# Performance work log

Hardware: AMD Instinct MI355X
Metric: run time of the kernel (lower is better)

The kernel has to match this reference:

```python
import jax, jax.numpy as jnp
import numpy as np

N = 50000      # nodes
E = 1600000    # edges (before self loops)
F = 128        # input_dim
H = 4          # num_heads
D = 32         # hidden_dim (per head)
B = 16         # graphs in batch
NEG_SLOPE = 0.2  # PyG GATv2Conv default negative_slope


def setup_inputs() -> dict:
    key = jax.random.key(0)
    ks = jax.random.split(key, 8)
    x = jax.random.normal(ks[0], (N, F), dtype=jnp.float32)
    edge_index = jax.random.randint(ks[1], (2, E), 0, N, dtype=jnp.int32)
    batch = jnp.sort(jax.random.randint(ks[2], (N,), 0, B, dtype=jnp.int32))
    s = 0.05
    W_l = jax.random.normal(ks[3], (F, H * D), dtype=jnp.float32) * s
    b_l = jnp.zeros((H * D,), dtype=jnp.float32)
    W_r = jax.random.normal(ks[4], (F, H * D), dtype=jnp.float32) * s
    b_r = jnp.zeros((H * D,), dtype=jnp.float32)
    att = jax.random.normal(ks[5], (H, D), dtype=jnp.float32) * s
    bias = jnp.zeros((H * D,), dtype=jnp.float32)
    return {"x": x, "edge_index": edge_index, "batch": batch,
            "W_l": W_l, "b_l": b_l, "W_r": W_r, "b_r": b_r,
            "att": att, "bias": bias}


def reference(x, edge_index, batch, W_l, b_l, W_r, b_r, att, bias):
    n = x.shape[0]
    # PyG GATv2Conv adds self loops by default
    loops = jnp.arange(n, dtype=edge_index.dtype)
    src = jnp.concatenate([edge_index[0], loops])  # message source j
    dst = jnp.concatenate([edge_index[1], loops])  # message target i

    xl = (x @ W_l + b_l).reshape(n, H, D)  # source transform
    xr = (x @ W_r + b_r).reshape(n, H, D)  # target transform

    # per-edge GATv2 attention logits: a^T LeakyReLU(xl_j + xr_i)
    m = xl[src] + xr[dst]                                   # [E+N, H, D]
    e = jnp.sum(jax.nn.leaky_relu(m, NEG_SLOPE) * att, -1)  # [E+N, H]

    # softmax over incoming edges of each destination node
    e_max = jax.ops.segment_max(e, dst, num_segments=n)
    ex = jnp.exp(e - e_max[dst])
    den = jax.ops.segment_sum(ex, dst, num_segments=n)
    alpha = ex / den[dst]                                   # [E+N, H]

    # weighted scatter-sum aggregation of source features
    out = jax.ops.segment_sum(alpha[..., None] * xl[src], dst, num_segments=n)
    out = out.reshape(n, H * D) + bias                      # concat heads + bias
    out = jax.nn.relu(out)

    # global max pool over nodes of each graph
    pooled = jax.ops.segment_max(out, batch, num_segments=B)
    pooled = jnp.where(jnp.isfinite(pooled), pooled, 0.0)   # guard empty graphs
    return pooled
```

## Files before the change

kernel.cpp:

```cpp
#include <hip/hip_runtime.h>

#define NN 50000
#define NE 1600000
#define FDIM 128
#define CDIM 128
#define NGRAPH 16
#define SLOPE 0.2f
#define CSTRIDE 96
#define BINSH 7
#define NBIN 391
#define EPB 6400
#define NB1 250
#define EPT 25
#define CAP 5120
#define POOL_NODES 64
#define POOL_NB ((NN + POOL_NODES - 1) / POOL_NODES)
#define TNB 782

__device__ __forceinline__ unsigned short f2bf(float f) {
    unsigned u = __float_as_uint(f);
    return (unsigned short)((u + 0x7FFFu + ((u >> 16) & 1u)) >> 16);
}
__device__ __forceinline__ unsigned packbf(float a, float b) {
    return (unsigned)f2bf(a) | ((unsigned)f2bf(b) << 16);
}
#define BFLO(u) __uint_as_float((u) << 16)
#define BFHI(u) __uint_as_float((u) & 0xffff0000u)

typedef __attribute__((ext_vector_type(8))) short short8;
typedef __attribute__((ext_vector_type(4))) float f32x4;
union FragU { uint4 u; short8 s; };

__global__ __launch_bounds__(256) void k_init(float* __restrict__ out,
                                              int* __restrict__ gbin_cnt) {
    int i = blockIdx.x * 256 + threadIdx.x;
    if (i < NGRAPH * CDIM) out[i] = 0.f;
    if (i < NBIN) gbin_cnt[i] = 0;
}

__global__ __launch_bounds__(256) void k_front(
    const float* __restrict__ x,
    const float* __restrict__ Wl, const float* __restrict__ bl,
    const float* __restrict__ Wr, const float* __restrict__ br,
    const int* __restrict__ src, const int* __restrict__ dst,
    int* __restrict__ gbin_cnt, unsigned* __restrict__ gstage,
    unsigned short* __restrict__ xlh, float* __restrict__ xr) {
    __shared__ __align__(16) char shraw[32768];
    const int tid = threadIdx.x;

    if (blockIdx.x < NB1) {
        int* bcnt = (int*)shraw;
        int* boff = bcnt + NBIN;
        int* gb   = boff + NBIN;
        int* sc   = gb + NBIN;
        unsigned* st = (unsigned*)(sc + 256);
        const int t  = tid;
        const int e0 = blockIdx.x * EPB;

        for (int b = t; b < NBIN; b += 256) bcnt[b] = 0;
        __syncthreads();

        unsigned sd[EPT]; int bn[EPT]; int pl[EPT];
#pragma unroll
        for (int k = 0; k < EPT; k++) {
            int e = e0 + k * 256 + t;
            int s = src[e], d = dst[e];
            bn[k] = d >> BINSH;
            sd[k] = (unsigned)s | ((unsigned)(d & 127) << 16)
                                | ((unsigned)bn[k] << 23);
            pl[k] = atomicAdd(&bcnt[bn[k]], 1);
        }
        __syncthreads();

        int c0 = (2*t     < NBIN) ? bcnt[2*t]     : 0;
        int c1 = (2*t + 1 < NBIN) ? bcnt[2*t + 1] : 0;
        int v  = c0 + c1;
        sc[t] = v; __syncthreads();
        for (int off = 1; off < 256; off <<= 1) {
            int add = (t >= off) ? sc[t - off] : 0;
            __syncthreads();
            sc[t] += add;
            __syncthreads();
        }
        int base = sc[t] - v;
        if (2*t     < NBIN) boff[2*t]     = base;
        if (2*t + 1 < NBIN) boff[2*t + 1] = base + c0;
        __syncthreads();

        for (int b = t; b < NBIN; b += 256) {
            int c = bcnt[b];
            gb[b] = (c > 0) ? atomicAdd(&gbin_cnt[b], c) : 0;
        }
#pragma unroll
        for (int k = 0; k < EPT; k++) st[boff[bn[k]] + pl[k]] = sd[k];
        __syncthreads();

        for (int idx = t; idx < EPB; idx += 256) {
            unsigned w = st[idx];
            int b = w >> 23;
            int p = gb[b] + (idx - boff[b]);
            if (p < CAP) gstage[(size_t)b * CAP + p] = w;
        }
    } else {
        uint4* wfrag = (uint4*)shraw;
        const int bid   = blockIdx.x - NB1;
        const int wv    = tid >> 6;
        const int lane  = tid & 63;
        const int quad  = lane >> 4;
        const int col   = lane & 15;
        const int node0 = bid * 64;
        const int nodeA = node0 + wv * 16 + col;
        const bool aval = nodeA < NN;

        FragU afrag[4];
#pragma unroll
        for (int kq = 0; kq < 4; kq++) {
            float4 lo = make_float4(0.f,0.f,0.f,0.f), hi = lo;
            if (aval) {
                const float* ap = &x[(size_t)nodeA * FDIM + kq * 32 + quad * 8];
                lo = *(const float4*)ap;
                hi = *(const float4*)(ap + 4);
            }
            afrag[kq].u.x = packbf(lo.x, lo.y);
            afrag[kq].u.y = packbf(lo.z, lo.w);
            afrag[kq].u.z = packbf(hi.x, hi.y);
            afrag[kq].u.w = packbf(hi.z, hi.w);
        }

        const int myrow0 = node0 + wv * 16 + quad * 4;

        for (int mat = 0; mat < 2; mat++) {
            const float* W  = mat ? Wr : Wl;
            const float* bb = mat ? br : bl;
            __syncthreads();
            for (int i = 0; i < 8; i++) {
                int C = i * 256 + tid;
                int ccol = C & 15, cq = (C >> 4) & 3, ckq = (C >> 6) & 3, cnt_ = C >> 8;
                const float* wp = &W[(size_t)(ckq * 32 + cq * 8) * CDIM + cnt_ * 16 + ccol];
                uint4 u;
                u.x = packbf(wp[0],        wp[CDIM]);
                u.y = packbf(wp[2*CDIM],   wp[3*CDIM]);
                u.z = packbf(wp[4*CDIM],   wp[5*CDIM]);
                u.w = packbf(wp[6*CDIM],   wp[7*CDIM]);
                wfrag[C] = u;
            }
            __syncthreads();

#pragma unroll
            for (int nt = 0; nt < 8; nt++) {
                f32x4 acc = {0.f, 0.f, 0.f, 0.f};
#pragma unroll
                for (int kq = 0; kq < 4; kq++) {
                    FragU bfr;
                    bfr.u = wfrag[(nt * 4 + kq) * 64 + lane];
                    acc = __builtin_amdgcn_mfma_f32_16x16x32_bf16(
                              afrag[kq].s, bfr.s, acc, 0, 0, 0);
                }
                int ch = nt * 16 + col;
                float bv = bb[ch];
                if (mat == 0) {
#pragma unroll
                    for (int r = 0; r < 4; r++) {
                        int node = myrow0 + r;
                        if (node < NN)
                            xlh[(size_t)node * CDIM + ch] = f2bf(acc[r] + bv);
                    }
                } else {
#pragma unroll
                    for (int r = 0; r < 4; r++) {
                        int node = myrow0 + r;
                        if (node < NN)
                            xr[(size_t)node * CDIM + ch] = acc[r] + bv;
                    }
                }
            }
        }
    }
}

__global__ __launch_bounds__(256) void k_csr(
    const int* __restrict__ gbin_cnt, const unsigned* __restrict__ gstage,
    int* __restrict__ cnt, unsigned short* __restrict__ colp) {
    __shared__ int nfill[128];
    __shared__ unsigned short crow[128 * CSTRIDE];
    const int bin = blockIdx.x;
    const int t   = threadIdx.x;
    const int n0  = bin << BINSH;
    const int nb  = min(128, NN - n0);
    const int m   = min(gbin_cnt[bin], CAP);

    if (t < 128) nfill[t] = 0;
    __syncthreads();

    for (int i = t; i < m; i += 256) {
        unsigned w = gstage[(size_t)bin * CAP + i];
        int dl = (w >> 16) & 127;
        int p  = atomicAdd(&nfill[dl], 1);
        if (p < CSTRIDE - 1) crow[dl * CSTRIDE + p] = (unsigned short)(w & 0xFFFF);
    }
    __syncthreads();

    if (t < nb) {
        int c = min(nfill[t], CSTRIDE - 1);
        crow[t * CSTRIDE + c] = (unsigned short)(n0 + t);
        cnt[n0 + t] = c + 1;
    }
    __syncthreads();

    unsigned* gout = (unsigned*)colp + (size_t)bin * (128 * CSTRIDE / 2);
    const unsigned* cin = (const unsigned*)crow;
    for (int idx = t; idx < 128 * CSTRIDE / 2; idx += 256) gout[idx] = cin[idx];
}

__device__ __forceinline__ void edge_body(
    const unsigned short* __restrict__ xlh, int j, int ch0,
    const float4& rx0, const float4& rx1,
    const float4& p0, const float4& p1,
    const float4& q0, const float4& q1,
    float& s, float* acc) {
    uint4 q = *(const uint4*)&xlh[(size_t)j * CDIM + ch0];
    float4 v0 = make_float4(BFLO(q.x), BFHI(q.x), BFLO(q.y), BFHI(q.y));
    float4 v1 = make_float4(BFLO(q.z), BFHI(q.z), BFLO(q.w), BFHI(q.w));
    float t0, d = 0.f;
    t0 = v0.x + rx0.x; d = fmaf(t0, p0.x, d); d = fmaf(fabsf(t0), q0.x, d);
    t0 = v0.y + rx0.y; d = fmaf(t0, p0.y, d); d = fmaf(fabsf(t0), q0.y, d);
    t0 = v0.z + rx0.z; d = fmaf(t0, p0.z, d); d = fmaf(fabsf(t0), q0.z, d);
    t0 = v0.w + rx0.w; d = fmaf(t0, p0.w, d); d = fmaf(fabsf(t0), q0.w, d);
    t0 = v1.x + rx1.x; d = fmaf(t0, p1.x, d); d = fmaf(fabsf(t0), q1.x, d);
    t0 = v1.y + rx1.y; d = fmaf(t0, p1.y, d); d = fmaf(fabsf(t0), q1.y, d);
    t0 = v1.z + rx1.z; d = fmaf(t0, p1.z, d); d = fmaf(fabsf(t0), q1.z, d);
    t0 = v1.w + rx1.w; d = fmaf(t0, p1.w, d); d = fmaf(fabsf(t0), q1.w, d);
    d += __shfl_xor(d, 1);
    d += __shfl_xor(d, 2);
    float w = __expf(d);
    s += w;
    acc[0] = fmaf(w, v0.x, acc[0]);
    acc[1] = fmaf(w, v0.y, acc[1]);
    acc[2] = fmaf(w, v0.z, acc[2]);
    acc[3] = fmaf(w, v0.w, acc[3]);
    acc[4] = fmaf(w, v1.x, acc[4]);
    acc[5] = fmaf(w, v1.y, acc[5]);
    acc[6] = fmaf(w, v1.z, acc[6]);
    acc[7] = fmaf(w, v1.w, acc[7]);
}

__global__ __launch_bounds__(256) void k_aggregate(
    const unsigned short* __restrict__ xlh, const float* __restrict__ xr,
    const float* __restrict__ att, const float* __restrict__ bias,
    const int* __restrict__ cnt, const unsigned short* __restrict__ colp,
    float* __restrict__ nodeout) {
    const int wave = blockIdx.x * 4 + (threadIdx.x >> 6);
    const int lane = threadIdx.x & 63;
    const int i     = wave;
    const size_t start = (size_t)i * CSTRIDE;
    const int deg   = cnt[i];
    const int grp   = lane >> 4;
    const int ch0   = (lane & 15) * 8;

    int cj0 = (int)colp[start + lane];
    int cj1 = 0;
    if (deg > 64) cj1 = (int)colp[start + 64 + lane];

    const float4 rx0 = *(const float4*)&xr[(size_t)i * CDIM + ch0];
    const float4 rx1 = *(const float4*)&xr[(size_t)i * CDIM + ch0 + 4];
    const float4 aa0 = *(const float4*)&att[ch0];
    const float4 aa1 = *(const float4*)&att[ch0 + 4];
    const float4 p0 = make_float4(0.6f*aa0.x, 0.6f*aa0.y, 0.6f*aa0.z, 0.6f*aa0.w);
    const float4 p1 = make_float4(0.6f*aa1.x, 0.6f*aa1.y, 0.6f*aa1.z, 0.6f*aa1.w);
    const float4 q0 = make_float4(0.4f*aa0.x, 0.4f*aa0.y, 0.4f*aa0.z, 0.4f*aa0.w);
    const float4 q1 = make_float4(0.4f*aa1.x, 0.4f*aa1.y, 0.4f*aa1.z, 0.4f*aa1.w);

    float s = 0.f;
    float acc[8];
#pragma unroll
    for (int k = 0; k < 8; k++) acc[k] = 0.f;

    const int full = deg >> 2;
    const int f0   = full < 16 ? full : 16;
#pragma unroll 2
    for (int t = 0; t < f0; t++) {
        int j = __shfl(cj0, t * 4 + grp);
        edge_body(xlh, j, ch0, rx0, rx1, p0, p1, q0, q1, s, acc);
    }
    for (int t = 16; t < full; t++) {
        int j = __shfl(cj1, t * 4 + grp - 64);
        edge_body(xlh, j, ch0, rx0, rx1, p0, p1, q0, q1, s, acc);
    }
    int e  = full * 4 + grp;
    int jt = (e < 64) ? __shfl(cj0, e) : __shfl(cj1, (e - 64) & 63);
    if (e < deg)
        edge_body(xlh, jt, ch0, rx0, rx1, p0, p1, q0, q1, s, acc);

#pragma unroll
    for (int dist = 16; dist <= 32; dist <<= 1) {
        s += __shfl_xor(s, dist);
#pragma unroll
        for (int k = 0; k < 8; k++) acc[k] += __shfl_xor(acc[k], dist);
    }

    if (grp == 0) {
        float inv = 1.f / s;
        float4 o0, o1;
        const float4 b0 = *(const float4*)&bias[ch0];
        const float4 b1 = *(const float4*)&bias[ch0 + 4];
        o0.x = fmaxf(fmaf(acc[0], inv, b0.x), 0.f);
        o0.y = fmaxf(fmaf(acc[1], inv, b0.y), 0.f);
        o0.z = fmaxf(fmaf(acc[2], inv, b0.z), 0.f);
        o0.w = fmaxf(fmaf(acc[3], inv, b0.w), 0.f);
        o1.x = fmaxf(fmaf(acc[4], inv, b1.x), 0.f);
        o1.y = fmaxf(fmaf(acc[5], inv, b1.y), 0.f);
        o1.z = fmaxf(fmaf(acc[6], inv, b1.z), 0.f);
        o1.w = fmaxf(fmaf(acc[7], inv, b1.w), 0.f);
        float* op = &nodeout[(size_t)i * CDIM + ch0];
        *(float4*)op       = o0;
        *(float4*)(op + 4) = o1;
    }
}

__global__ __launch_bounds__(256) void k_pool(
    const float* __restrict__ nodeout, const int* __restrict__ batch,
    float* __restrict__ out) {
    const int tid  = threadIdx.x;
    const int c4   = (tid & 31) * 4;
    const int nl   = tid >> 5;
    const int base = blockIdx.x * POOL_NODES;
    float4 mx = make_float4(0.f, 0.f, 0.f, 0.f);
    int cur = -1;
#pragma unroll
    for (int k = 0; k < POOL_NODES / 8; k++) {
        int node = base + k * 8 + nl;
        if (node >= NN) break;
        int g = batch[node];
        if (g != cur) {
            if (cur >= 0) {
                int* op = (int*)&out[cur * CDIM + c4];
                if (mx.x > 0.f) atomicMax(op,     __float_as_int(mx.x));
                if (mx.y > 0.f) atomicMax(op + 1, __float_as_int(mx.y));
                if (mx.z > 0.f) atomicMax(op + 2, __float_as_int(mx.z));
                if (mx.w > 0.f) atomicMax(op + 3, __float_as_int(mx.w));
            }
            cur = g;
            mx = make_float4(0.f, 0.f, 0.f, 0.f);
        }
        float4 v = *(const float4*)&nodeout[(size_t)node * CDIM + c4];
        mx.x = fmaxf(mx.x, v.x);
        mx.y = fmaxf(mx.y, v.y);
        mx.z = fmaxf(mx.z, v.z);
        mx.w = fmaxf(mx.w, v.w);
    }
    if (cur >= 0) {
        int* op = (int*)&out[cur * CDIM + c4];
        if (mx.x > 0.f) atomicMax(op,     __float_as_int(mx.x));
        if (mx.y > 0.f) atomicMax(op + 1, __float_as_int(mx.y));
        if (mx.z > 0.f) atomicMax(op + 2, __float_as_int(mx.z));
        if (mx.w > 0.f) atomicMax(op + 3, __float_as_int(mx.w));
    }
}

extern "C" void kernel_launch(void* const* d_in, const int* in_sizes, int n_in,
                              void* d_out, int out_size, void* d_ws, size_t ws_size,
                              hipStream_t stream) {
    const float* x     = (const float*)d_in[0];
    const int*   ei    = (const int*)d_in[1];
    const int*   batch = (const int*)d_in[2];
    const float* Wl    = (const float*)d_in[3];
    const float* bl    = (const float*)d_in[4];
    const float* Wr    = (const float*)d_in[5];
    const float* br    = (const float*)d_in[6];
    const float* att   = (const float*)d_in[7];
    const float* bias  = (const float*)d_in[8];
    float* out = (float*)d_out;

    char* w = (char*)d_ws;
    float*          xr       = (float*)w;          w += (size_t)NN * CDIM * 4;
    float*          nodeout  = (float*)w;          w += (size_t)NN * CDIM * 4;
    unsigned short* xlh      = (unsigned short*)w; w += (size_t)NN * CDIM * 2;
    int*            cnt      = (int*)w;            w += (size_t)NN * 4;
    unsigned short* colp     = (unsigned short*)w; w += (size_t)NBIN * 128 * CSTRIDE * 2;
    unsigned*       gstage   = (unsigned*)w;       w += (size_t)NBIN * CAP * 4;
    int*            gbin_cnt = (int*)w;            w += (size_t)NBIN * 4;

    const int* src = ei;
    const int* dst = ei + NE;

    k_init<<<10, 256, 0, stream>>>(out, gbin_cnt);
    k_front<<<NB1 + TNB, 256, 0, stream>>>(x, Wl, bl, Wr, br,
                                           src, dst, gbin_cnt, gstage, xlh, xr);
    k_csr<<<NBIN, 256, 0, stream>>>(gbin_cnt, gstage, cnt, colp);
    k_aggregate<<<NN / 4, 256, 0, stream>>>(xlh, xr, att, bias,
                                            cnt, colp, nodeout);
    k_pool<<<POOL_NB, 256, 0, stream>>>(nodeout, batch, out);
}
```

Before: 237.3 us.

## Fuse CSR build, attention aggregation and max-pool into one back-half kernel

Replaces the separate CSR, aggregate and pool kernels with one kernel. Each 512-thread block builds the adjacency for half of a 128-node bin in shared memory, then aggregates those nodes wave by wave and folds the ReLU outputs straight into per-graph max atomics. This drops the global round trips for the column list, degree counts and the full node-output matrix, along with two kernel launches. In exchange every bin's staging buffer is scanned twice, once per half, and each wave handles eight nodes serially, which gives fewer independent waves for hiding gather latency.

Result: slower. 318.2 us (+34.0%).

```diff
diff --git a/kernel.cpp b/kernel.cpp
--- a/kernel.cpp
+++ b/kernel.cpp
@@ -13,8 +13,6 @@
 #define NB1 250
 #define EPT 25
 #define CAP 5120
-#define POOL_NODES 64
-#define POOL_NB ((NN + POOL_NODES - 1) / POOL_NODES)
 #define TNB 782
 
 __device__ __forceinline__ unsigned short f2bf(float f) {
@@ -178,182 +176,190 @@
     }
 }
 
-__global__ __launch_bounds__(256) void k_csr(
+__global__ __launch_bounds__(512) void k_backhalf(
+    const unsigned short* __restrict__ xlh, const float* __restrict__ xr,
+    const float* __restrict__ att, const float* __restrict__ bias,
+    const int* __restrict__ batch,
     const int* __restrict__ gbin_cnt, const unsigned* __restrict__ gstage,
-    int* __restrict__ cnt, unsigned short* __restrict__ colp) {
-    __shared__ int nfill[128];
-    __shared__ unsigned short crow[128 * CSTRIDE];
-    const int bin = blockIdx.x;
-    const int t   = threadIdx.x;
-    const int n0  = bin << BINSH;
-    const int nb  = min(128, NN - n0);
+    float* __restrict__ out) {
+    __shared__ int nfill[64];
+    __shared__ unsigned short crow[64 * CSTRIDE];
+    const int bin = blockIdx.x >> 1;
+    const int h   = blockIdx.x & 1;
+    const int tid = threadIdx.x;
+    const int n0  = (bin << BINSH) + h * 64;
+    const int nb  = min(64, NN - n0);
     const int m   = min(gbin_cnt[bin], CAP);
 
-    if (t < 128) nfill[t] = 0;
+    if (tid < 64) nfill[tid] = 0;
     __syncthreads();
 
-    for (int i = t; i < m; i += 256) {
+    for (int i = tid; i < m; i += 512) {
         unsigned w = gstage[(size_t)bin * CAP + i];
         int dl = (w >> 16) & 127;
-        int p  = atomicAdd(&nfill[dl], 1);
-        if (p < CSTRIDE - 1) crow[dl * CSTRIDE + p] = (unsigned short)(w & 0xFFFF);
+        if ((dl >> 6) == h) {
+            int r = dl & 63;
+            int p = atomicAdd(&nfill[r], 1);
+            if (p < CSTRIDE - 1) crow[r * CSTRIDE + p] = (unsigned short)(w & 0xFFFF);
+        }
     }
     __syncthreads();
-
-    if (t < nb) {
-        int c = min(nfill[t], CSTRIDE - 1);
-        crow[t * CSTRIDE + c] = (unsigned short)(n0 + t);
-        cnt[n0 + t] = c + 1;
+    if (tid < nb) {
+        int c = min(nfill[tid], CSTRIDE - 1);
+        crow[tid * CSTRIDE + c] = (unsigned short)(n0 + tid);
+        nfill[tid] = c + 1;
     }
     __syncthreads();
 
-    unsigned* gout = (unsigned*)colp + (size_t)bin * (128 * CSTRIDE / 2);
-    const unsigned* cin = (const unsigned*)crow;
-    for (int idx = t; idx < 128 * CSTRIDE / 2; idx += 256) gout[idx] = cin[idx];
-}
-
-__device__ __forceinline__ void edge_body(
-    const unsigned short* __restrict__ xlh, int j, int ch0,
-    const float4& rx0, const float4& rx1,
-    const float4& p0, const float4& p1,
-    const float4& q0, const float4& q1,
-    float& s, float* acc) {
-    uint4 q = *(const uint4*)&xlh[(size_t)j * CDIM + ch0];
-    float4 v0 = make_float4(BFLO(q.x), BFHI(q.x), BFLO(q.y), BFHI(q.y));
-    float4 v1 = make_float4(BFLO(q.z), BFHI(q.z), BFLO(q.w), BFHI(q.w));
-    float t0, d = 0.f;
-    t0 = v0.x + rx0.x; d = fmaf(t0, p0.x, d); d = fmaf(fabsf(t0), q0.x, d);
-    t0 = v0.y + rx0.y; d = fmaf(t0, p0.y, d); d = fmaf(fabsf(t0), q0.y, d);
-    t0 = v0.z + rx0.z; d = fmaf(t0, p0.z, d); d = fmaf(fabsf(t0), q0.z, d);
-    t0 = v0.w + rx0.w; d = fmaf(t0, p0.w, d); d = fmaf(fabsf(t0), q0.w, d);
-    t0 = v1.x + rx1.x; d = fmaf(t0, p1.x, d); d = fmaf(fabsf(t0), q1.x, d);
-    t0 = v1.y + rx1.y; d = fmaf(t0, p1.y, d); d = fmaf(fabsf(t0), q1.y, d);
-    t0 = v1.z + rx1.z; d = fmaf(t0, p1.z, d); d = fmaf(fabsf(t0), q1.z, d);
-    t0 = v1.w + rx1.w; d = fmaf(t0, p1.w, d); d = fmaf(fabsf(t0), q1.w, d);
-    d += __shfl_xor(d, 1);
-    d += __shfl_xor(d, 2);
-    float w = __expf(d);
-    s += w;
-    acc[0] = fmaf(w, v0.x, acc[0]);
-    acc[1] = fmaf(w, v0.y, acc[1]);
-    acc[2] = fmaf(w, v0.z, acc[2]);
-    acc[3] = fmaf(w, v0.w, acc[3]);
-    acc[4] = fmaf(w, v1.x, acc[4]);
-    acc[5] = fmaf(w, v1.y, acc[5]);
-    acc[6] = fmaf(w, v1.z, acc[6]);
-    acc[7] = fmaf(w, v1.w, acc[7]);
-}
-
-__global__ __launch_bounds__(256) void k_aggregate(
-    const unsigned short* __restrict__ xlh, const float* __restrict__ xr,
-    const float* __restrict__ att, const float* __restrict__ bias,
-    const int* __restrict__ cnt, const unsigned short* __restrict__ colp,
-    float* __restrict__ nodeout) {
-    const int wave = blockIdx.x * 4 + (threadIdx.x >> 6);
-    const int lane = threadIdx.x & 63;
-    const int i     = wave;
-    const size_t start = (size_t)i * CSTRIDE;
-    const int deg   = cnt[i];
-    const int grp   = lane >> 4;
-    const int ch0   = (lane & 15) * 8;
-
-    int cj0 = (int)colp[start + lane];
-    int cj1 = 0;
-    if (deg > 64) cj1 = (int)colp[start + 64 + lane];
-
-    const float4 rx0 = *(const float4*)&xr[(size_t)i * CDIM + ch0];
-    const float4 rx1 = *(const float4*)&xr[(size_t)i * CDIM + ch0 + 4];
+    const int wv   = tid >> 6;
+    const int lane = tid & 63;
+    const int grp  = lane >> 4;
+    const int ch0  = (lane & 15) * 8;
+
     const float4 aa0 = *(const float4*)&att[ch0];
     const float4 aa1 = *(const float4*)&att[ch0 + 4];
     const float4 p0 = make_float4(0.6f*aa0.x, 0.6f*aa0.y, 0.6f*aa0.z, 0.6f*aa0.w);
     const float4 p1 = make_float4(0.6f*aa1.x, 0.6f*aa1.y, 0.6f*aa1.z, 0.6f*aa1.w);
     const float4 q0 = make_float4(0.4f*aa0.x, 0.4f*aa0.y, 0.4f*aa0.z, 0.4f*aa0.w);
     const float4 q1 = make_float4(0.4f*aa1.x, 0.4f*aa1.y, 0.4f*aa1.z, 0.4f*aa1.w);
-
-    float s = 0.f;
-    float acc[8];
-#pragma unroll
-    for (int k = 0; k < 8; k++) acc[k] = 0.f;
-
-    const int full = deg >> 2;
-    const int f0   = full < 16 ? full : 16;
+    const float4 b0 = *(const float4*)&bias[ch0];
+    const float4 b1 = *(const float4*)&bias[ch0 + 4];
+
+    float pmax[8];
+#pragma unroll
+    for (int k = 0; k < 8; k++) pmax[k] = 0.f;
+    int curg = -1;
+
+    for (int k = 0; k < 8; k++) {
+        int r = wv * 8 + k;
+        if (r >= nb) break;
+        const int node = n0 + r;
+        const int deg  = nfill[r];
+        int cj0 = (int)crow[r * CSTRIDE + lane];
+        int cj1 = (int)crow[r * CSTRIDE + 64 + (lane & 31)];
+        const float4 rx0 = *(const float4*)&xr[(size_t)node * CDIM + ch0];
+        const float4 rx1 = *(const float4*)&xr[(size_t)node * CDIM + ch0 + 4];
+
+        float s = 0.f;
+        float acc[8];
+#pragma unroll
+        for (int j = 0; j < 8; j++) acc[j] = 0.f;
+
+        const int full = deg >> 2;
+        const int f0   = full < 16 ? full : 16;
 #pragma unroll 2
-    for (int t = 0; t < f0; t++) {
-        int j = __shfl(cj0, t * 4 + grp);
-        edge_body(xlh, j, ch0, rx0, rx1, p0, p1, q0, q1, s, acc);
-    }
-    for (int t = 16; t < full; t++) {
-        int j = __shfl(cj1, t * 4 + grp - 64);
-        edge_body(xlh, j, ch0, rx0, rx1, p0, p1, q0, q1, s, acc);
-    }
-    int e  = full * 4 + grp;
-    int jt = (e < 64) ? __shfl(cj0, e) : __shfl(cj1, (e - 64) & 63);
-    if (e < deg)
-        edge_body(xlh, jt, ch0, rx0, rx1, p0, p1, q0, q1, s, acc);
-
-#pragma unroll
-    for (int dist = 16; dist <= 32; dist <<= 1) {
-        s += __shfl_xor(s, dist);
-#pragma unroll
-        for (int k = 0; k < 8; k++) acc[k] += __shfl_xor(acc[k], dist);
-    }
-
-    if (grp == 0) {
+        for (int t = 0; t < f0; t++) {
+            int j = __shfl(cj0, t * 4 + grp);
+            {
+                uint4 q = *(const uint4*)&xlh[(size_t)j * CDIM + ch0];
+                float4 v0 = make_float4(BFLO(q.x), BFHI(q.x), BFLO(q.y), BFHI(q.y));
+                float4 v1 = make_float4(BFLO(q.z), BFHI(q.z), BFLO(q.w), BFHI(q.w));
+                float t0, d = 0.f;
+                t0 = v0.x + rx0.x; d = fmaf(t0, p0.x, d); d = fmaf(fabsf(t0), q0.x, d);
+                t0 = v0.y + rx0.y; d = fmaf(t0, p0.y, d); d = fmaf(fabsf(t0), q0.y, d);
+                t0 = v0.z + rx0.z; d = fmaf(t0, p0.z, d); d = fmaf(fabsf(t0), q0.z, d);
+                t0 = v0.w + rx0.w; d = fmaf(t0, p0.w, d); d = fmaf(fabsf(t0), q0.w, d);
+                t0 = v1.x + rx1.x; d = fmaf(t0, p1.x, d); d = fmaf(fabsf(t0), q1.x, d);
+                t0 = v1.y + rx1.y; d = fmaf(t0, p1.y, d); d = fmaf(fabsf(t0), q1.y, d);
+                t0 = v1.z + rx1.z; d = fmaf(t0, p1.z, d); d = fmaf(fabsf(t0), q1.z, d);
+                t0 = v1.w + rx1.w; d = fmaf(t0, p1.w, d); d = fmaf(fabsf(t0), q1.w, d);
+                d += __shfl_xor(d, 1);
+                d += __shfl_xor(d, 2);
+                float w = __expf(d);
+                s += w;
+                acc[0] = fmaf(w, v0.x, acc[0]); acc[1] = fmaf(w, v0.y, acc[1]);
+                acc[2] = fmaf(w, v0.z, acc[2]); acc[3] = fmaf(w, v0.w, acc[3]);
+                acc[4] = fmaf(w, v1.x, acc[4]); acc[5] = fmaf(w, v1.y, acc[5]);
+                acc[6] = fmaf(w, v1.z, acc[6]); acc[7] = fmaf(w, v1.w, acc[7]);
+            }
+        }
+        for (int t = 16; t < full; t++) {
+            int j = __shfl(cj1, t * 4 + grp - 64);
+            uint4 q = *(const uint4*)&xlh[(size_t)j * CDIM + ch0];
+            float4 v0 = make_float4(BFLO(q.x), BFHI(q.x), BFLO(q.y), BFHI(q.y));
+            float4 v1 = make_float4(BFLO(q.z), BFHI(q.z), BFLO(q.w), BFHI(q.w));
+            float t0, d = 0.f;
+            t0 = v0.x + rx0.x; d = fmaf(t0, p0.x, d); d = fmaf(fabsf(t0), q0.x, d);
+            t0 = v0.y + rx0.y; d = fmaf(t0, p0.y, d); d = fmaf(fabsf(t0), q0.y, d);
+            t0 = v0.z + rx0.z; d = fmaf(t0, p0.z, d); d = fmaf(fabsf(t0), q0.z, d);
+            t0 = v0.w + rx0.w; d = fmaf(t0, p0.w, d); d = fmaf(fabsf(t0), q0.w, d);
+            t0 = v1.x + rx1.x; d = fmaf(t0, p1.x, d); d = fmaf(fabsf(t0), q1.x, d);
+            t0 = v1.y + rx1.y; d = fmaf(t0, p1.y, d); d = fmaf(fabsf(t0), q1.y, d);
+            t0 = v1.z + rx1.z; d = fmaf(t0, p1.z, d); d = fmaf(fabsf(t0), q1.z, d);
+            t0 = v1.w + rx1.w; d = fmaf(t0, p1.w, d); d = fmaf(fabsf(t0), q1.w, d);
+            d += __shfl_xor(d, 1);
+            d += __shfl_xor(d, 2);
+            float w = __expf(d);
+            s += w;
+            acc[0] = fmaf(w, v0.x, acc[0]); acc[1] = fmaf(w, v0.y, acc[1]);
+            acc[2] = fmaf(w, v0.z, acc[2]); acc[3] = fmaf(w, v0.w, acc[3]);
+            acc[4] = fmaf(w, v1.x, acc[4]); acc[5] = fmaf(w, v1.y, acc[5]);
+            acc[6] = fmaf(w, v1.z, acc[6]); acc[7] = fmaf(w, v1.w, acc[7]);
+        }
+        int e  = full * 4 + grp;
+        int jt = (e < 64) ? __shfl(cj0, e) : __shfl(cj1, (e - 64) & 63);
+        if (e < deg) {
+            uint4 q = *(const uint4*)&xlh[(size_t)jt * CDIM + ch0];
+            float4 v0 = make_float4(BFLO(q.x), BFHI(q.x), BFLO(q.y), BFHI(q.y));
+            float4 v1 = make_float4(BFLO(q.z), BFHI(q.z), BFLO(q.w), BFHI(q.w));
+            float t0, d = 0.f;
+            t0 = v0.x + rx0.x; d = fmaf(t0, p0.x, d); d = fmaf(fabsf(t0), q0.x, d);
+            t0 = v0.y + rx0.y; d = fmaf(t0, p0.y, d); d = fmaf(fabsf(t0), q0.y, d);
+            t0 = v0.z + rx0.z; d = fmaf(t0, p0.z, d); d = fmaf(fabsf(t0), q0.z, d);
+            t0 = v0.w + rx0.w; d = fmaf(t0, p0.w, d); d = fmaf(fabsf(t0), q0.w, d);
+            t0 = v1.x + rx1.x; d = fmaf(t0, p1.x, d); d = fmaf(fabsf(t0), q1.x, d);
+            t0 = v1.y + rx1.y; d = fmaf(t0, p1.y, d); d = fmaf(fabsf(t0), q1.y, d);
+            t0 = v1.z + rx1.z; d = fmaf(t0, p1.z, d); d = fmaf(fabsf(t0), q1.z, d);
+            t0 = v1.w + rx1.w; d = fmaf(t0, p1.w, d); d = fmaf(fabsf(t0), q1.w, d);
+            d += __shfl_xor(d, 1);
+            d += __shfl_xor(d, 2);
+            float w = __expf(d);
+            s += w;
+            acc[0] = fmaf(w, v0.x, acc[0]); acc[1] = fmaf(w, v0.y, acc[1]);
+            acc[2] = fmaf(w, v0.z, acc[2]); acc[3] = fmaf(w, v0.w, acc[3]);
+            acc[4] = fmaf(w, v1.x, acc[4]); acc[5] = fmaf(w, v1.y, acc[5]);
+            acc[6] = fmaf(w, v1.z, acc[6]); acc[7] = fmaf(w, v1.w, acc[7]);
+        }
+
+#pragma unroll
+        for (int dist = 16; dist <= 32; dist <<= 1) {
+            s += __shfl_xor(s, dist);
+#pragma unroll
+            for (int j = 0; j < 8; j++) acc[j] += __shfl_xor(acc[j], dist);
+        }
+
         float inv = 1.f / s;
-        float4 o0, o1;
-        const float4 b0 = *(const float4*)&bias[ch0];
-        const float4 b1 = *(const float4*)&bias[ch0 + 4];
-        o0.x = fmaxf(fmaf(acc[0], inv, b0.x), 0.f);
-        o0.y = fmaxf(fmaf(acc[1], inv, b0.y), 0.f);
-        o0.z = fmaxf(fmaf(acc[2], inv, b0.z), 0.f);
-        o0.w = fmaxf(fmaf(acc[3], inv, b0.w), 0.f);
-        o1.x = fmaxf(fmaf(acc[4], inv, b1.x), 0.f);
-        o1.y = fmaxf(fmaf(acc[5], inv, b1.y), 0.f);
-        o1.z = fmaxf(fmaf(acc[6], inv, b1.z), 0.f);
-        o1.w = fmaxf(fmaf(acc[7], inv, b1.w), 0.f);
-        float* op = &nodeout[(size_t)i * CDIM + ch0];
-        *(float4*)op       = o0;
-        *(float4*)(op + 4) = o1;
-    }
-}
-
-__global__ __launch_bounds__(256) void k_pool(
-    const float* __restrict__ nodeout, const int* __restrict__ batch,
-    float* __restrict__ out) {
-    const int tid  = threadIdx.x;
-    const int c4   = (tid & 31) * 4;
-    const int nl   = tid >> 5;
-    const int base = blockIdx.x * POOL_NODES;
-    float4 mx = make_float4(0.f, 0.f, 0.f, 0.f);
-    int cur = -1;
-#pragma unroll
-    for (int k = 0; k < POOL_NODES / 8; k++) {
-        int node = base + k * 8 + nl;
-        if (node >= NN) break;
+        float o[8];
+        o[0] = fmaxf(fmaf(acc[0], inv, b0.x), 0.f);
+        o[1] = fmaxf(fmaf(acc[1], inv, b0.y), 0.f);
+        o[2] = fmaxf(fmaf(acc[2], inv, b0.z), 0.f);
+        o[3] = fmaxf(fmaf(acc[3], inv, b0.w), 0.f);
+        o[4] = fmaxf(fmaf(acc[4], inv, b1.x), 0.f);
+        o[5] = fmaxf(fmaf(acc[5], inv, b1.y), 0.f);
+        o[6] = fmaxf(fmaf(acc[6], inv, b1.z), 0.f);
+        o[7] = fmaxf(fmaf(acc[7], inv, b1.w), 0.f);
+
         int g = batch[node];
-        if (g != cur) {
-            if (cur >= 0) {
-                int* op = (int*)&out[cur * CDIM + c4];
-                if (mx.x > 0.f) atomicMax(op,     __float_as_int(mx.x));
-                if (mx.y > 0.f) atomicMax(op + 1, __float_as_int(mx.y));
-                if (mx.z > 0.f) atomicMax(op + 2, __float_as_int(mx.z));
-                if (mx.w > 0.f) atomicMax(op + 3, __float_as_int(mx.w));
-            }
-            cur = g;
-            mx = make_float4(0.f, 0.f, 0.f, 0.f);
-        }
-        float4 v = *(const float4*)&nodeout[(size_t)node * CDIM + c4];
-        mx.x = fmaxf(mx.x, v.x);
-        mx.y = fmaxf(mx.y, v.y);
-        mx.z = fmaxf(mx.z, v.z);
-        mx.w = fmaxf(mx.w, v.w);
-    }
-    if (cur >= 0) {
-        int* op = (int*)&out[cur * CDIM + c4];
-        if (mx.x > 0.f) atomicMax(op,     __float_as_int(mx.x));
-        if (mx.y > 0.f) atomicMax(op + 1, __float_as_int(mx.y));
-        if (mx.z > 0.f) atomicMax(op + 2, __float_as_int(mx.z));
-        if (mx.w > 0.f) atomicMax(op + 3, __float_as_int(mx.w));
+        if (g != curg) {
+            if (curg >= 0 && grp == 0) {
+                int* op = (int*)&out[curg * CDIM + ch0];
+#pragma unroll
+                for (int j = 0; j < 8; j++)
+                    if (pmax[j] > 0.f) atomicMax(op + j, __float_as_int(pmax[j]));
+            }
+            curg = g;
+#pragma unroll
+            for (int j = 0; j < 8; j++) pmax[j] = 0.f;
+        }
+#pragma unroll
+        for (int j = 0; j < 8; j++) pmax[j] = fmaxf(pmax[j], o[j]);
+    }
+
+    if (curg >= 0 && grp == 0) {
+        int* op = (int*)&out[curg * CDIM + ch0];
+#pragma unroll
+        for (int j = 0; j < 8; j++)
+            if (pmax[j] > 0.f) atomicMax(op + j, __float_as_int(pmax[j]));
     }
 }
 
@@ -373,10 +379,7 @@
 
     char* w = (char*)d_ws;
     float*          xr       = (float*)w;          w += (size_t)NN * CDIM * 4;
-    float*          nodeout  = (float*)w;          w += (size_t)NN * CDIM * 4;
     unsigned short* xlh      = (unsigned short*)w; w += (size_t)NN * CDIM * 2;
-    int*            cnt      = (int*)w;            w += (size_t)NN * 4;
-    unsigned short* colp     = (unsigned short*)w; w += (size_t)NBIN * 128 * CSTRIDE * 2;
     unsigned*       gstage   = (unsigned*)w;       w += (size_t)NBIN * CAP * 4;
     int*            gbin_cnt = (int*)w;            w += (size_t)NBIN * 4;
 
@@ -386,8 +389,6 @@
     k_init<<<10, 256, 0, stream>>>(out, gbin_cnt);
     k_front<<<NB1 + TNB, 256, 0, stream>>>(x, Wl, bl, Wr, br,
                                            src, dst, gbin_cnt, gstage, xlh, xr);
-    k_csr<<<NBIN, 256, 0, stream>>>(gbin_cnt, gstage, cnt, colp);
-    k_aggregate<<<NN / 4, 256, 0, stream>>>(xlh, xr, att, bias,
-                                            cnt, colp, nodeout);
-    k_pool<<<POOL_NB, 256, 0, stream>>>(nodeout, batch, out);
-}
+    k_backhalf<<<NBIN * 2, 512, 0, stream>>>(xlh, xr, att, bias, batch,
+                                             gbin_cnt, gstage, out);
+}
```
